# Kernel optimization log

Hardware: AMD Instinct MI355X
Metric: run time of the kernel (lower is better)

The kernel has to match this reference:

```python
import jax, jax.numpy as jnp
import numpy as np

B, C_IN, H, W = 1, 3, 96, 96
NB_CLASSES = 21
NB_ITER = 5
THETA_ALPHA, THETA_BETA, THETA_GAMMA = 160.0, 3.0, 3.0


def setup_inputs() -> dict:
    key = jax.random.key(0)
    ks = jax.random.split(key, 8)
    image = jax.random.uniform(ks[0], (B, C_IN, H, W), jnp.float32)
    net_w = jax.random.normal(ks[1], (NB_CLASSES, C_IN, 3, 3), jnp.float32) * 0.1
    net_b = jax.random.normal(ks[2], (NB_CLASSES,), jnp.float32) * 0.01
    sp_w = jax.random.normal(ks[3], (NB_CLASSES, NB_CLASSES), jnp.float32) * 0.1
    sp_b = jnp.zeros((NB_CLASSES,), jnp.float32)
    bl_w = jax.random.normal(ks[4], (NB_CLASSES, NB_CLASSES), jnp.float32) * 0.1
    bl_b = jnp.zeros((NB_CLASSES,), jnp.float32)
    comp_w = jax.random.normal(ks[5], (NB_CLASSES, NB_CLASSES), jnp.float32) * 0.1
    comp_b = jnp.zeros((NB_CLASSES,), jnp.float32)
    return {"image": image, "net_w": net_w, "net_b": net_b,
            "sp_w": sp_w, "sp_b": sp_b, "bl_w": bl_w, "bl_b": bl_b,
            "comp_w": comp_w, "comp_b": comp_b}


def _gauss_kernel(feat):
    # feat: [B, N, D] -> K[B, N, N] = exp(-||f_i - f_j||^2 / 2)
    sq = jnp.sum(feat * feat, axis=-1)
    d2 = sq[:, :, None] + sq[:, None, :] - 2.0 * jnp.einsum('bnd,bmd->bnm', feat, feat)
    return jnp.exp(-0.5 * jnp.maximum(d2, 0.0))


def _crf_forward(image, net_w, net_b, sp_w, sp_b, bl_w, bl_b, comp_w, comp_b):
    b, c_in, h, w = image.shape
    n = h * w
    nb_classes = net_w.shape[0]
    # unary network: 3x3 same conv
    unaries = jax.lax.conv_general_dilated(
        image, net_w, (1, 1), 'SAME',
        dimension_numbers=('NCHW', 'OIHW', 'NCHW')) + net_b[None, :, None, None]
    # feature-space Gaussian kernels (exact form the permutohedral lattice approximates)
    yy, xx = jnp.meshgrid(jnp.arange(h, dtype=jnp.float32),
                          jnp.arange(w, dtype=jnp.float32), indexing='ij')
    pos = jnp.stack([xx.ravel(), yy.ravel()], axis=-1)          # [N, 2]
    pos_b = jnp.broadcast_to(pos, (b, n, 2))
    img_flat = image.reshape(b, c_in, n).transpose(0, 2, 1)      # [B, N, Cin]
    k_sp = _gauss_kernel(pos_b / THETA_GAMMA)                    # spatial kernel
    k_bl = _gauss_kernel(jnp.concatenate(
        [pos_b / THETA_ALPHA, img_flat / THETA_BETA], axis=-1))  # bilateral kernel
    norm_sp = k_sp.sum(-1)                                       # [B, N]
    norm_bl = k_bl.sum(-1)

    def filt(k, norm, s):
        return jnp.einsum('bnm,bcm->bcn', k, s) / norm[:, None, :]

    u = unaries.reshape(b, nb_classes, n)
    q = u
    s = jax.nn.softmax(q, axis=1)
    for _ in range(NB_ITER):
        sp = filt(k_sp, norm_sp, s)
        bl = filt(k_bl, norm_bl, s)
        mp = (jnp.einsum('oc,bcn->bon', sp_w, sp) + sp_b[None, :, None]
              + jnp.einsum('oc,bcn->bon', bl_w, bl) + bl_b[None, :, None])
        pairwise = jnp.einsum('oc,bcn->bon', comp_w, mp) + comp_b[None, :, None]
        q = u - pairwise
        s = jax.nn.softmax(q, axis=1)
    return s.reshape(b, nb_classes, h, w)


def reference(image, net_w, net_b, sp_w, sp_b, bl_w, bl_b, comp_w, comp_b):
    return _crf_forward(image, net_w, net_b, sp_w, sp_b, bl_w, bl_b, comp_w, comp_b)
```

## Files before the change

kernel.cpp:

```cpp
#include <hip/hip_runtime.h>

#define NPIX 9216
#define IMH 96
#define IMW 96
#define NC 21
#define NCH 22
#define NMON 126
#define RAD 15
#define NITER 5
#define MSZ 2772
#define SP 97
#define QP 25
#define NT 1024

__constant__ float GW[16] = {
    1.0f, 0.945959f, 0.800737f, 0.606531f, 0.411112f, 0.249352f,
    0.135335f, 0.0657285f, 0.0285655f, 0.0111090f, 0.00386592f,
    0.00120386f, 0.000335463f, 8.36523e-05f, 1.86640e-05f, 3.72665e-06f};

__constant__ float d_bk[5] = {1.000000f, 0.998959f, 0.509936f, 0.139441f, 0.070024f};

__device__ __forceinline__ void a_part(
    const float* s_sh, const float* __restrict__ phi, int base,
    float* __restrict__ Mdst, float* __restrict__ sx_out, int tid)
{
    for (int t = tid; t < MSZ; t += NT) {
        const int m = t / NCH, c = t % NCH;
        const float* pr = phi + (size_t)m * NPIX + base;
        const float* sr = s_sh + c * SP;
        float acc = 0.f;
        #pragma unroll
        for (int p4 = 0; p4 < 24; p4++) {
            const float4 pv = *(const float4*)(pr + p4 * 4);
            acc += pv.x * sr[p4 * 4] + pv.y * sr[p4 * 4 + 1] +
                   pv.z * sr[p4 * 4 + 2] + pv.w * sr[p4 * 4 + 3];
        }
        atomicAdd(&Mdst[t], acc);
    }
    for (int t = tid; t < NCH * 96; t += NT) {
        const int px = t % 96, ch = t / 96;
        const float* sr = s_sh + ch * SP;
        float a = GW[0] * sr[px];
        #pragma unroll
        for (int d = 1; d <= RAD; d++) {
            const float l = (px - d >= 0) ? sr[px - d] : 0.f;
            const float r = (px + d < 96) ? sr[px + d] : 0.f;
            a = fmaf(GW[d], l + r, a);
        }
        sx_out[(size_t)ch * NPIX + base + px] = a;
    }
}

__global__ __launch_bounds__(NT) void prep_kernel(
    const float* __restrict__ img, const float* __restrict__ net_w,
    const float* __restrict__ net_b,
    float* __restrict__ u, float* __restrict__ phi,
    float* __restrict__ M0, float* __restrict__ sx_out)
{
    __shared__ float wsh[588];
    __shared__ float sg_sh[NMON];
    __shared__ float ex_sh[NMON * 5];
    __shared__ float pt[96 * QP];
    __shared__ float env[96];
    __shared__ float cq[96 * QP];
    __shared__ float s_sh[NCH * SP];
    const int tid = threadIdx.x, row = blockIdx.x, base = row * 96;

    for (int i = tid; i < 567; i += NT) wsh[i] = net_w[i];
    if (tid < 21) wsh[567 + tid] = net_b[tid];
    if (tid < NMON) {
        const int m = tid;
        int e1 = 0, e2 = 0, e3 = 0, e4 = 0, e5 = 0, cnt = 0;
        bool done = false;
        for (int a = 0; a <= 4 && !done; a++)
            for (int b2 = 0; b2 <= 4 - a && !done; b2++)
                for (int c = 0; c <= 4 - a - b2 && !done; c++)
                    for (int d = 0; d <= 4 - a - b2 - c && !done; d++) {
                        const int rem = 4 - a - b2 - c - d;
                        if (m - cnt <= rem) {
                            e1 = a; e2 = b2; e3 = c; e4 = d; e5 = m - cnt;
                            done = true;
                        } else cnt += rem + 1;
                    }
        const float fact[5] = {1.f, 1.f, 2.f, 6.f, 24.f};
        const int k = e1 + e2 + e3 + e4 + e5;
        sg_sh[m] = sqrtf(d_bk[k] * fact[k] /
                         (fact[e1] * fact[e2] * fact[e3] * fact[e4] * fact[e5]));
        ex_sh[m * 5 + 0] = (float)e1; ex_sh[m * 5 + 1] = (float)e2;
        ex_sh[m * 5 + 2] = (float)e3; ex_sh[m * 5 + 3] = (float)e4;
        ex_sh[m * 5 + 4] = (float)e5;
    }
    __syncthreads();

    for (int t = tid; t < 96 * NC; t += NT) {
        const int px = t % 96, o = t / 96;
        float acc = wsh[567 + o];
        for (int ci = 0; ci < 3; ci++)
            for (int ky = 0; ky < 3; ky++)
                for (int kx = 0; kx < 3; kx++) {
                    const int ii = row + ky - 1, jj = px + kx - 1;
                    float v = 0.f;
                    if (ii >= 0 && ii < IMH && jj >= 0 && jj < IMW)
                        v = img[ci * NPIX + ii * IMW + jj];
                    acc = fmaf(v, wsh[o * 27 + (ci * 3 + ky) * 3 + kx], acc);
                }
        cq[px * QP + o] = acc;
        u[(size_t)o * NPIX + base + px] = acc;
    }
    if (tid < 96) {
        const float fv[5] = {(float)tid * (1.0f / 160.0f),
                             (float)row * (1.0f / 160.0f),
                             img[0 * NPIX + base + tid] * (1.0f / 3.0f),
                             img[1 * NPIX + base + tid] * (1.0f / 3.0f),
                             img[2 * NPIX + base + tid] * (1.0f / 3.0f)};
        env[tid] = __expf(-0.5f * (fv[0]*fv[0] + fv[1]*fv[1] + fv[2]*fv[2] +
                                   fv[3]*fv[3] + fv[4]*fv[4]));
        #pragma unroll
        for (int v = 0; v < 5; v++) {
            float p = 1.f;
            #pragma unroll
            for (int e = 0; e < 5; e++) { pt[tid * QP + v * 5 + e] = p; p *= fv[v]; }
        }
    }
    __syncthreads();
    if (tid < 96) {
        float a[NC];
        #pragma unroll
        for (int o = 0; o < NC; o++) a[o] = cq[tid * QP + o];
        float mx = a[0];
        #pragma unroll
        for (int o = 1; o < NC; o++) mx = fmaxf(mx, a[o]);
        float sum = 0.f;
        #pragma unroll
        for (int o = 0; o < NC; o++) { a[o] = __expf(a[o] - mx); sum += a[o]; }
        const float inv = 1.f / sum;
        #pragma unroll
        for (int o = 0; o < NC; o++) s_sh[o * SP + tid] = a[o] * inv;
        s_sh[21 * SP + tid] = 1.f;
    }
    for (int t = tid; t < NMON * 96; t += NT) {
        const int px = t % 96, m = t / 96;
        float p = env[px] * sg_sh[m];
        p *= pt[px * QP + 0 + (int)ex_sh[m * 5 + 0]];
        p *= pt[px * QP + 5 + (int)ex_sh[m * 5 + 1]];
        p *= pt[px * QP + 10 + (int)ex_sh[m * 5 + 2]];
        p *= pt[px * QP + 15 + (int)ex_sh[m * 5 + 3]];
        p *= pt[px * QP + 20 + (int)ex_sh[m * 5 + 4]];
        phi[(size_t)m * NPIX + base + px] = p;
    }
    __syncthreads();

    a_part(s_sh, phi, base, M0, sx_out, tid);
}

__global__ __launch_bounds__(NT) void kba_kernel(
    const float* __restrict__ sx_in, float* __restrict__ sx_out,
    const float* __restrict__ phi,
    const float* __restrict__ Mcur, float* __restrict__ Mnext,
    float* __restrict__ Mzero, const float* __restrict__ u,
    const float* __restrict__ sp_w, const float* __restrict__ sp_b,
    const float* __restrict__ bl_w, const float* __restrict__ bl_b,
    const float* __restrict__ comp_w, const float* __restrict__ comp_b,
    float* __restrict__ out, int write_out, int doA)
{
    __shared__ float Msh[NMON * 24];
    __shared__ float cy_sh[96 * QP];
    __shared__ float blv_sh[96 * QP];
    __shared__ float mp_sh[96 * QP];
    __shared__ float s_sh[NCH * SP];
    __shared__ float wsh[1449];
    const int tid = threadIdx.x, row = blockIdx.x, base = row * 96;

    for (int t = tid; t < NMON * 24; t += NT) {
        const int m = t / 24, c = t % 24;
        Msh[t] = (c < NCH) ? Mcur[m * NCH + c] : 0.f;
    }
    for (int i = tid; i < 441; i += NT) {
        wsh[i] = sp_w[i]; wsh[441 + i] = bl_w[i]; wsh[882 + i] = comp_w[i];
    }
    if (tid < 21) {
        wsh[1323 + tid] = sp_b[tid]; wsh[1344 + tid] = bl_b[tid];
        wsh[1365 + tid] = comp_b[tid];
    }
    {
        const int idx = row * 29 + tid;
        if (tid < 29 && idx < MSZ) Mzero[idx] = 0.f;
    }
    for (int t = tid; t < NCH * 96; t += NT) {
        const int px = t % 96, ch = t / 96;
        const float* plane = sx_in + (size_t)ch * NPIX;
        float a = GW[0] * plane[base + px];
        #pragma unroll
        for (int d = 1; d <= RAD; d++) {
            const float tp = (row - d >= 0) ? plane[base - d * IMW + px] : 0.f;
            const float bt = (row + d < IMH) ? plane[base + d * IMW + px] : 0.f;
            a = fmaf(GW[d], tp + bt, a);
        }
        cy_sh[px * QP + ch] = a;
    }
    __syncthreads();

    for (int t = tid; t < 96 * 8; t += NT) {
        const int px = t % 96, c0 = (t / 96) * 3;
        float a0 = 0.f, a1 = 0.f, a2 = 0.f;
        for (int m = 0; m < NMON; m++) {
            const float ph = phi[(size_t)m * NPIX + base + px];
            const float* Mr = Msh + m * 24 + c0;
            a0 = fmaf(ph, Mr[0], a0);
            a1 = fmaf(ph, Mr[1], a1);
            a2 = fmaf(ph, Mr[2], a2);
        }
        blv_sh[px * QP + c0] = a0;
        if (c0 + 1 < NCH) blv_sh[px * QP + c0 + 1] = a1;
        if (c0 + 2 < NCH) blv_sh[px * QP + c0 + 2] = a2;
    }
    __syncthreads();

    for (int t = tid; t < 96 * NC; t += NT) {
        const int px = t % 96, o = t / 96;
        const float* cyr = cy_sh + px * QP;
        const float* blr = blv_sh + px * QP;
        float dS = 0.f, dB = 0.f;
        #pragma unroll
        for (int c = 0; c < NC; c++) {
            dS = fmaf(wsh[o * NC + c], cyr[c], dS);
            dB = fmaf(wsh[441 + o * NC + c], blr[c], dB);
        }
        mp_sh[px * QP + o] = wsh[1323 + o] + wsh[1344 + o] +
                             dS / cyr[21] + dB / blr[21];
    }
    __syncthreads();

    for (int t = tid; t < 96 * NC; t += NT) {
        const int px = t % 96, o = t / 96;
        const float* mpr = mp_sh + px * QP;
        float d = wsh[1365 + o];
        #pragma unroll
        for (int c = 0; c < NC; c++) d = fmaf(wsh[882 + o * NC + c], mpr[c], d);
        cy_sh[px * QP + o] = u[(size_t)o * NPIX + base + px] - d;
    }
    __syncthreads();

    if (tid < 96) {
        float q[NC];
        #pragma unroll
        for (int o = 0; o < NC; o++) q[o] = cy_sh[tid * QP + o];
        float mx = q[0];
        #pragma unroll
        for (int o = 1; o < NC; o++) mx = fmaxf(mx, q[o]);
        float sum = 0.f;
        #pragma unroll
        for (int o = 0; o < NC; o++) { q[o] = __expf(q[o] - mx); sum += q[o]; }
        const float inv = 1.f / sum;
        #pragma unroll
        for (int o = 0; o < NC; o++) {
            const float sv = q[o] * inv;
            s_sh[o * SP + tid] = sv;
            if (write_out) out[(size_t)o * NPIX + base + tid] = sv;
        }
        s_sh[21 * SP + tid] = 1.f;
    }
    __syncthreads();

    if (doA) a_part(s_sh, phi, base, Mnext, sx_out, tid);
}

extern "C" void kernel_launch(void* const* d_in, const int* in_sizes, int n_in,
                              void* d_out, int out_size, void* d_ws, size_t ws_size,
                              hipStream_t stream) {
    const float* img    = (const float*)d_in[0];
    const float* net_w  = (const float*)d_in[1];
    const float* net_b  = (const float*)d_in[2];
    const float* sp_w   = (const float*)d_in[3];
    const float* sp_b   = (const float*)d_in[4];
    const float* bl_w   = (const float*)d_in[5];
    const float* bl_b   = (const float*)d_in[6];
    const float* comp_w = (const float*)d_in[7];
    const float* comp_b = (const float*)d_in[8];

    float* M   = (float*)d_ws;
    float* u   = M + 3 * MSZ;
    float* sx  = u + (size_t)NC * NPIX;
    float* phi = sx + (size_t)2 * NCH * NPIX;

    float* out = (float*)d_out;

    hipMemsetAsync(M, 0, 3 * MSZ * sizeof(float), stream);
    prep_kernel<<<dim3(96), dim3(NT), 0, stream>>>(
        img, net_w, net_b, u, phi, M, sx);
    for (int it = 0; it < NITER; it++) {
        float* Mcur  = M + (it % 3) * MSZ;
        float* Mnext = M + ((it + 1) % 3) * MSZ;
        float* Mzero = M + ((it + 2) % 3) * MSZ;
        kba_kernel<<<dim3(96), dim3(NT), 0, stream>>>(
            sx + (size_t)(it & 1) * NCH * NPIX,
            sx + (size_t)((it + 1) & 1) * NCH * NPIX,
            phi, Mcur, Mnext, Mzero, u,
            sp_w, sp_b, bl_w, bl_b, comp_w, comp_b,
            out, it == NITER - 1 ? 1 : 0, it < NITER - 1 ? 1 : 0);
    }
}
```

Baseline: 238.2 us.

## Split each image row across two blocks with halo recompute

```diff
diff --git a/kernel.cpp b/kernel.cpp
--- a/kernel.cpp
+++ b/kernel.cpp
@@ -9,9 +9,10 @@
 #define RAD 15
 #define NITER 5
 #define MSZ 2772
-#define SP 97
+#define HP 78
+#define SP2 79
 #define QP 25
-#define NT 1024
+#define NT 512
 
 __constant__ float GW[16] = {
     1.0f, 0.945959f, 0.800737f, 0.606531f, 0.411112f, 0.249352f,
@@ -19,37 +20,6 @@
     0.00120386f, 0.000335463f, 8.36523e-05f, 1.86640e-05f, 3.72665e-06f};
 
 __constant__ float d_bk[5] = {1.000000f, 0.998959f, 0.509936f, 0.139441f, 0.070024f};
-
-__device__ __forceinline__ void a_part(
-    const float* s_sh, const float* __restrict__ phi, int base,
-    float* __restrict__ Mdst, float* __restrict__ sx_out, int tid)
-{
-    for (int t = tid; t < MSZ; t += NT) {
-        const int m = t / NCH, c = t % NCH;
-        const float* pr = phi + (size_t)m * NPIX + base;
-        const float* sr = s_sh + c * SP;
-        float acc = 0.f;
-        #pragma unroll
-        for (int p4 = 0; p4 < 24; p4++) {
-            const float4 pv = *(const float4*)(pr + p4 * 4);
-            acc += pv.x * sr[p4 * 4] + pv.y * sr[p4 * 4 + 1] +
-                   pv.z * sr[p4 * 4 + 2] + pv.w * sr[p4 * 4 + 3];
-        }
-        atomicAdd(&Mdst[t], acc);
-    }
-    for (int t = tid; t < NCH * 96; t += NT) {
-        const int px = t % 96, ch = t / 96;
-        const float* sr = s_sh + ch * SP;
-        float a = GW[0] * sr[px];
-        #pragma unroll
-        for (int d = 1; d <= RAD; d++) {
-            const float l = (px - d >= 0) ? sr[px - d] : 0.f;
-            const float r = (px + d < 96) ? sr[px + d] : 0.f;
-            a = fmaf(GW[d], l + r, a);
-        }
-        sx_out[(size_t)ch * NPIX + base + px] = a;
-    }
-}
 
 __global__ __launch_bounds__(NT) void prep_kernel(
     const float* __restrict__ img, const float* __restrict__ net_w,
@@ -60,11 +30,14 @@
     __shared__ float wsh[588];
     __shared__ float sg_sh[NMON];
     __shared__ float ex_sh[NMON * 5];
-    __shared__ float pt[96 * QP];
-    __shared__ float env[96];
-    __shared__ float cq[96 * QP];
-    __shared__ float s_sh[NCH * SP];
-    const int tid = threadIdx.x, row = blockIdx.x, base = row * 96;
+    __shared__ float pt[HP * QP];
+    __shared__ float env[HP];
+    __shared__ float cq[HP * QP];
+    __shared__ float s_sh[NCH * SP2];
+    __shared__ float phi_sh[NMON * 48];
+    const int tid = threadIdx.x;
+    const int row = blockIdx.x >> 1, h = blockIdx.x & 1;
+    const int base = row * 96, x0 = h * 48 - 15;
 
     for (int i = tid; i < 567; i += NT) wsh[i] = net_w[i];
     if (tid < 21) wsh[567 + tid] = net_b[tid];
@@ -92,65 +65,95 @@
     }
     __syncthreads();
 
-    for (int t = tid; t < 96 * NC; t += NT) {
-        const int px = t % 96, o = t / 96;
+    for (int t = tid; t < HP * NC; t += NT) {
+        const int l = t % HP, o = t / HP;
+        const int gpx = x0 + l;
+        if (gpx < 0 || gpx >= 96) continue;
         float acc = wsh[567 + o];
         for (int ci = 0; ci < 3; ci++)
             for (int ky = 0; ky < 3; ky++)
                 for (int kx = 0; kx < 3; kx++) {
-                    const int ii = row + ky - 1, jj = px + kx - 1;
+                    const int ii = row + ky - 1, jj = gpx + kx - 1;
                     float v = 0.f;
                     if (ii >= 0 && ii < IMH && jj >= 0 && jj < IMW)
                         v = img[ci * NPIX + ii * IMW + jj];
                     acc = fmaf(v, wsh[o * 27 + (ci * 3 + ky) * 3 + kx], acc);
                 }
-        cq[px * QP + o] = acc;
-        u[(size_t)o * NPIX + base + px] = acc;
-    }
-    if (tid < 96) {
-        const float fv[5] = {(float)tid * (1.0f / 160.0f),
-                             (float)row * (1.0f / 160.0f),
-                             img[0 * NPIX + base + tid] * (1.0f / 3.0f),
-                             img[1 * NPIX + base + tid] * (1.0f / 3.0f),
-                             img[2 * NPIX + base + tid] * (1.0f / 3.0f)};
-        env[tid] = __expf(-0.5f * (fv[0]*fv[0] + fv[1]*fv[1] + fv[2]*fv[2] +
-                                   fv[3]*fv[3] + fv[4]*fv[4]));
+        cq[l * QP + o] = acc;
+        if (l >= 15 && l < 63) u[(size_t)o * NPIX + base + gpx] = acc;
+    }
+    if (tid < HP) {
+        const int gpx = x0 + tid;
+        if (gpx >= 0 && gpx < 96) {
+            const float fv[5] = {(float)gpx * (1.0f / 160.0f),
+                                 (float)row * (1.0f / 160.0f),
+                                 img[0 * NPIX + base + gpx] * (1.0f / 3.0f),
+                                 img[1 * NPIX + base + gpx] * (1.0f / 3.0f),
+                                 img[2 * NPIX + base + gpx] * (1.0f / 3.0f)};
+            env[tid] = __expf(-0.5f * (fv[0]*fv[0] + fv[1]*fv[1] + fv[2]*fv[2] +
+                                       fv[3]*fv[3] + fv[4]*fv[4]));
+            #pragma unroll
+            for (int v = 0; v < 5; v++) {
+                float p = 1.f;
+                #pragma unroll
+                for (int e = 0; e < 5; e++) { pt[tid * QP + v * 5 + e] = p; p *= fv[v]; }
+            }
+        }
+    }
+    __syncthreads();
+    if (tid < HP) {
+        const int gpx = x0 + tid;
+        if (gpx < 0 || gpx >= 96) {
+            #pragma unroll
+            for (int o = 0; o < NCH; o++) s_sh[o * SP2 + tid] = 0.f;
+        } else {
+            float a[NC];
+            #pragma unroll
+            for (int o = 0; o < NC; o++) a[o] = cq[tid * QP + o];
+            float mx = a[0];
+            #pragma unroll
+            for (int o = 1; o < NC; o++) mx = fmaxf(mx, a[o]);
+            float sum = 0.f;
+            #pragma unroll
+            for (int o = 0; o < NC; o++) { a[o] = __expf(a[o] - mx); sum += a[o]; }
+            const float inv = 1.f / sum;
+            #pragma unroll
+            for (int o = 0; o < NC; o++) s_sh[o * SP2 + tid] = a[o] * inv;
+            s_sh[21 * SP2 + tid] = 1.f;
+        }
+    }
+    for (int t = tid; t < NMON * 48; t += NT) {
+        const int m = t / 48, k = t % 48;
+        const int l = k + 15;
+        float p = env[l] * sg_sh[m];
+        p *= pt[l * QP + 0 + (int)ex_sh[m * 5 + 0]];
+        p *= pt[l * QP + 5 + (int)ex_sh[m * 5 + 1]];
+        p *= pt[l * QP + 10 + (int)ex_sh[m * 5 + 2]];
+        p *= pt[l * QP + 15 + (int)ex_sh[m * 5 + 3]];
+        p *= pt[l * QP + 20 + (int)ex_sh[m * 5 + 4]];
+        phi_sh[t] = p;
+        phi[(size_t)m * NPIX + base + h * 48 + k] = p;
+    }
+    __syncthreads();
+
+    for (int t = tid; t < MSZ; t += NT) {
+        const int m = t / NCH, c = t % NCH;
+        const float* pr = phi_sh + m * 48;
+        const float* sr = s_sh + c * SP2 + 15;
+        float acc = 0.f;
+        #pragma unroll 8
+        for (int k = 0; k < 48; k++) acc = fmaf(pr[k], sr[k], acc);
+        atomicAdd(&M0[t], acc);
+    }
+    for (int t = tid; t < NCH * 48; t += NT) {
+        const int ch = t / 48, k = t % 48, l = k + 15;
+        const float* sr = s_sh + ch * SP2;
+        float a = GW[0] * sr[l];
         #pragma unroll
-        for (int v = 0; v < 5; v++) {
-            float p = 1.f;
-            #pragma unroll
-            for (int e = 0; e < 5; e++) { pt[tid * QP + v * 5 + e] = p; p *= fv[v]; }
-        }
-    }
-    __syncthreads();
-    if (tid < 96) {
-        float a[NC];
-        #pragma unroll
-        for (int o = 0; o < NC; o++) a[o] = cq[tid * QP + o];
-        float mx = a[0];
-        #pragma unroll
-        for (int o = 1; o < NC; o++) mx = fmaxf(mx, a[o]);
-        float sum = 0.f;
-        #pragma unroll
-        for (int o = 0; o < NC; o++) { a[o] = __expf(a[o] - mx); sum += a[o]; }
-        const float inv = 1.f / sum;
-        #pragma unroll
-        for (int o = 0; o < NC; o++) s_sh[o * SP + tid] = a[o] * inv;
-        s_sh[21 * SP + tid] = 1.f;
-    }
-    for (int t = tid; t < NMON * 96; t += NT) {
-        const int px = t % 96, m = t / 96;
-        float p = env[px] * sg_sh[m];
-        p *= pt[px * QP + 0 + (int)ex_sh[m * 5 + 0]];
-        p *= pt[px * QP + 5 + (int)ex_sh[m * 5 + 1]];
-        p *= pt[px * QP + 10 + (int)ex_sh[m * 5 + 2]];
-        p *= pt[px * QP + 15 + (int)ex_sh[m * 5 + 3]];
-        p *= pt[px * QP + 20 + (int)ex_sh[m * 5 + 4]];
-        phi[(size_t)m * NPIX + base + px] = p;
-    }
-    __syncthreads();
-
-    a_part(s_sh, phi, base, M0, sx_out, tid);
+        for (int d = 1; d <= RAD; d++)
+            a = fmaf(GW[d], sr[l - d] + sr[l + d], a);
+        sx_out[(size_t)ch * NPIX + base + h * 48 + k] = a;
+    }
 }
 
 __global__ __launch_bounds__(NT) void kba_kernel(
@@ -164,12 +167,14 @@
     float* __restrict__ out, int write_out, int doA)
 {
     __shared__ float Msh[NMON * 24];
-    __shared__ float cy_sh[96 * QP];
-    __shared__ float blv_sh[96 * QP];
-    __shared__ float mp_sh[96 * QP];
-    __shared__ float s_sh[NCH * SP];
+    __shared__ float cy_sh[HP * QP];
+    __shared__ float blv_sh[HP * QP];
+    __shared__ float mp_sh[HP * QP];
+    __shared__ float s_sh[NCH * SP2];
     __shared__ float wsh[1449];
-    const int tid = threadIdx.x, row = blockIdx.x, base = row * 96;
+    const int tid = threadIdx.x;
+    const int row = blockIdx.x >> 1, h = blockIdx.x & 1;
+    const int base = row * 96, x0 = h * 48 - 15;
 
     for (int t = tid; t < NMON * 24; t += NT) {
         const int m = t / 24, c = t % 24;
@@ -183,86 +188,124 @@
         wsh[1365 + tid] = comp_b[tid];
     }
     {
-        const int idx = row * 29 + tid;
-        if (tid < 29 && idx < MSZ) Mzero[idx] = 0.f;
-    }
-    for (int t = tid; t < NCH * 96; t += NT) {
-        const int px = t % 96, ch = t / 96;
+        const int idx = blockIdx.x * 15 + tid;
+        if (tid < 15 && idx < MSZ) Mzero[idx] = 0.f;
+    }
+    for (int t = tid; t < NCH * HP; t += NT) {
+        const int l = t % HP, ch = t / HP;
+        const int gpx = x0 + l;
+        if (gpx < 0 || gpx >= 96) continue;
         const float* plane = sx_in + (size_t)ch * NPIX;
-        float a = GW[0] * plane[base + px];
+        float a = GW[0] * plane[base + gpx];
         #pragma unroll
         for (int d = 1; d <= RAD; d++) {
-            const float tp = (row - d >= 0) ? plane[base - d * IMW + px] : 0.f;
-            const float bt = (row + d < IMH) ? plane[base + d * IMW + px] : 0.f;
+            const float tp = (row - d >= 0) ? plane[base - d * IMW + gpx] : 0.f;
+            const float bt = (row + d < IMH) ? plane[base + d * IMW + gpx] : 0.f;
             a = fmaf(GW[d], tp + bt, a);
         }
-        cy_sh[px * QP + ch] = a;
-    }
-    __syncthreads();
-
-    for (int t = tid; t < 96 * 8; t += NT) {
-        const int px = t % 96, c0 = (t / 96) * 3;
+        cy_sh[l * QP + ch] = a;
+    }
+    __syncthreads();
+
+    for (int t = tid; t < HP * 8; t += NT) {
+        const int l = t % HP, c0 = (t / HP) * 3;
+        const int gpx = x0 + l;
+        if (gpx < 0 || gpx >= 96) continue;
         float a0 = 0.f, a1 = 0.f, a2 = 0.f;
         for (int m = 0; m < NMON; m++) {
-            const float ph = phi[(size_t)m * NPIX + base + px];
+            const float ph = phi[(size_t)m * NPIX + base + gpx];
             const float* Mr = Msh + m * 24 + c0;
             a0 = fmaf(ph, Mr[0], a0);
             a1 = fmaf(ph, Mr[1], a1);
             a2 = fmaf(ph, Mr[2], a2);
         }
-        blv_sh[px * QP + c0] = a0;
-        if (c0 + 1 < NCH) blv_sh[px * QP + c0 + 1] = a1;
-        if (c0 + 2 < NCH) blv_sh[px * QP + c0 + 2] = a2;
-    }
-    __syncthreads();
-
-    for (int t = tid; t < 96 * NC; t += NT) {
-        const int px = t % 96, o = t / 96;
-        const float* cyr = cy_sh + px * QP;
-        const float* blr = blv_sh + px * QP;
+        blv_sh[l * QP + c0] = a0;
+        if (c0 + 1 < NCH) blv_sh[l * QP + c0 + 1] = a1;
+        if (c0 + 2 < NCH) blv_sh[l * QP + c0 + 2] = a2;
+    }
+    __syncthreads();
+
+    for (int t = tid; t < HP * NC; t += NT) {
+        const int l = t % HP, o = t / HP;
+        const int gpx = x0 + l;
+        if (gpx < 0 || gpx >= 96) continue;
+        const float* cyr = cy_sh + l * QP;
+        const float* blr = blv_sh + l * QP;
         float dS = 0.f, dB = 0.f;
         #pragma unroll
         for (int c = 0; c < NC; c++) {
             dS = fmaf(wsh[o * NC + c], cyr[c], dS);
             dB = fmaf(wsh[441 + o * NC + c], blr[c], dB);
         }
-        mp_sh[px * QP + o] = wsh[1323 + o] + wsh[1344 + o] +
-                             dS / cyr[21] + dB / blr[21];
-    }
-    __syncthreads();
-
-    for (int t = tid; t < 96 * NC; t += NT) {
-        const int px = t % 96, o = t / 96;
-        const float* mpr = mp_sh + px * QP;
+        mp_sh[l * QP + o] = wsh[1323 + o] + wsh[1344 + o] +
+                            dS / cyr[21] + dB / blr[21];
+    }
+    __syncthreads();
+
+    for (int t = tid; t < HP * NC; t += NT) {
+        const int l = t % HP, o = t / HP;
+        const int gpx = x0 + l;
+        if (gpx < 0 || gpx >= 96) continue;
+        const float* mpr = mp_sh + l * QP;
         float d = wsh[1365 + o];
         #pragma unroll
         for (int c = 0; c < NC; c++) d = fmaf(wsh[882 + o * NC + c], mpr[c], d);
-        cy_sh[px * QP + o] = u[(size_t)o * NPIX + base + px] - d;
-    }
-    __syncthreads();
-
-    if (tid < 96) {
-        float q[NC];
-        #pragma unroll
-        for (int o = 0; o < NC; o++) q[o] = cy_sh[tid * QP + o];
-        float mx = q[0];
-        #pragma unroll
-        for (int o = 1; o < NC; o++) mx = fmaxf(mx, q[o]);
-        float sum = 0.f;
-        #pragma unroll
-        for (int o = 0; o < NC; o++) { q[o] = __expf(q[o] - mx); sum += q[o]; }
-        const float inv = 1.f / sum;
-        #pragma unroll
-        for (int o = 0; o < NC; o++) {
-            const float sv = q[o] * inv;
-            s_sh[o * SP + tid] = sv;
-            if (write_out) out[(size_t)o * NPIX + base + tid] = sv;
-        }
-        s_sh[21 * SP + tid] = 1.f;
-    }
-    __syncthreads();
-
-    if (doA) a_part(s_sh, phi, base, Mnext, sx_out, tid);
+        cy_sh[l * QP + o] = u[(size_t)o * NPIX + base + gpx] - d;
+    }
+    __syncthreads();
+
+    if (tid < HP) {
+        const int gpx = x0 + tid;
+        if (gpx < 0 || gpx >= 96) {
+            #pragma unroll
+            for (int o = 0; o < NCH; o++) s_sh[o * SP2 + tid] = 0.f;
+        } else {
+            float q[NC];
+            #pragma unroll
+            for (int o = 0; o < NC; o++) q[o] = cy_sh[tid * QP + o];
+            float mx = q[0];
+            #pragma unroll
+            for (int o = 1; o < NC; o++) mx = fmaxf(mx, q[o]);
+            float sum = 0.f;
+            #pragma unroll
+            for (int o = 0; o < NC; o++) { q[o] = __expf(q[o] - mx); sum += q[o]; }
+            const float inv = 1.f / sum;
+            #pragma unroll
+            for (int o = 0; o < NC; o++) {
+                const float sv = q[o] * inv;
+                s_sh[o * SP2 + tid] = sv;
+                if (write_out && tid >= 15 && tid < 63)
+                    out[(size_t)o * NPIX + base + gpx] = sv;
+            }
+            s_sh[21 * SP2 + tid] = 1.f;
+        }
+    }
+    __syncthreads();
+
+    if (doA) {
+        for (int t = tid; t < MSZ; t += NT) {
+            const int m = t / NCH, c = t % NCH;
+            const float* pr = phi + (size_t)m * NPIX + base + h * 48;
+            const float* sr = s_sh + c * SP2 + 15;
+            float acc = 0.f;
+            #pragma unroll
+            for (int p4 = 0; p4 < 12; p4++) {
+                const float4 pv = *(const float4*)(pr + p4 * 4);
+                acc += pv.x * sr[p4 * 4] + pv.y * sr[p4 * 4 + 1] +
+                       pv.z * sr[p4 * 4 + 2] + pv.w * sr[p4 * 4 + 3];
+            }
+            atomicAdd(&Mnext[t], acc);
+        }
+        for (int t = tid; t < NCH * 48; t += NT) {
+            const int ch = t / 48, k = t % 48, l = k + 15;
+            const float* sr = s_sh + ch * SP2;
+            float a = GW[0] * sr[l];
+            #pragma unroll
+            for (int d = 1; d <= RAD; d++)
+                a = fmaf(GW[d], sr[l - d] + sr[l + d], a);
+            sx_out[(size_t)ch * NPIX + base + h * 48 + k] = a;
+        }
+    }
 }
 
 extern "C" void kernel_launch(void* const* d_in, const int* in_sizes, int n_in,
@@ -286,13 +329,13 @@
     float* out = (float*)d_out;
 
     hipMemsetAsync(M, 0, 3 * MSZ * sizeof(float), stream);
-    prep_kernel<<<dim3(96), dim3(NT), 0, stream>>>(
+    prep_kernel<<<dim3(192), dim3(NT), 0, stream>>>(
         img, net_w, net_b, u, phi, M, sx);
     for (int it = 0; it < NITER; it++) {
         float* Mcur  = M + (it % 3) * MSZ;
         float* Mnext = M + ((it + 1) % 3) * MSZ;
         float* Mzero = M + ((it + 2) % 3) * MSZ;
-        kba_kernel<<<dim3(96), dim3(NT), 0, stream>>>(
+        kba_kernel<<<dim3(192), dim3(NT), 0, stream>>>(
             sx + (size_t)(it & 1) * NCH * NPIX,
             sx + (size_t)((it + 1) & 1) * NCH * NPIX,
             phi, Mcur, Mnext, Mzero, u,
```

Result: no change. 241.3 us (+1.3%).
